# Kernel tuning notes

Measured on AMD Instinct MI355X. Metric: run time of the kernel, lower is better.

The kernel has to match this reference:

```python
import jax, jax.numpy as jnp
import numpy as np

ORDER = 12      # Coef_num in the original
BLOCK = 1024
N_FFT = 2046    # torch.stft(n_fft=2046) -> 1024 onesided bins
HOP = 511       # torch default n_fft // 4
WORN = 1024
G1, G2 = 0.92, 0.6


def burg_lpc(y):
    """Burg's method LPC (exactly librosa.lpc), vectorized over blocks. y: [B, N] -> [B, ORDER+1]."""
    ar = jnp.zeros((y.shape[0], ORDER + 1), y.dtype).at[:, 0].set(1.0)
    f = y[:, 1:]
    b = y[:, :-1]
    den = jnp.sum(f * f, -1) + jnp.sum(b * b, -1)
    for i in range(ORDER):
        k = -2.0 * jnp.sum(b * f, -1) / den                     # reflection coeff [B]
        js = np.arange(1, i + 2)
        ar = ar.at[:, js].set(ar[:, js] + k[:, None] * ar[:, i - js + 1])
        f_new = f + k[:, None] * b
        b = b + k[:, None] * f
        f = f_new
        den = (1.0 - k * k) * den - b[:, -1] ** 2 - f[:, 0] ** 2
        f = f[:, 1:]
        b = b[:, :-1]
    return ar


def perceptual_weights(y):
    """Stacked |freqz| weight matrix [n_blocks*11, 1024], matching the original append order."""
    n_blocks = y.shape[0] // BLOCK
    yb = y[: n_blocks * BLOCK].reshape(n_blocks, BLOCK)
    lpc = burg_lpc(yb)[:, :ORDER]                               # original drops coeff index 12
    j = np.arange(ORDER)
    a1 = (lpc * (G1 ** j)).astype(jnp.complex64)                # denominator coeffs (bandwidth-expanded)
    a2 = (lpc * (G2 ** j)).astype(jnp.complex64)                # numerator coeffs
    omega = jnp.pi * jnp.arange(WORN) / WORN                    # freqz worN=1024 digital freqs
    E = jnp.exp(-1j * omega[:, None] * j[None, :]).astype(jnp.complex64)   # [F, 12]
    # freqz is called inside the k1 loop: at step k1 only coeffs 0..k1 are filled -> triangular mask
    M = jnp.asarray(j[None, :] <= np.arange(1, ORDER)[:, None], jnp.complex64)  # [11, 12]
    num = jnp.einsum('bj,kj,fj->bkf', a2, M, E)
    den = jnp.einsum('bj,kj,fj->bkf', a1, M, E)
    return jnp.abs(num / den).reshape(n_blocks * (ORDER - 1), WORN)


def stft_mag(x):
    """torch.stft(x, n_fft=2046, center=True, reflect pad, rect window, onesided) magnitude -> [1024, n_frames]."""
    pad = N_FFT // 2
    xp = jnp.pad(x, (pad, pad), mode='reflect')
    n_frames = 1 + x.shape[0] // HOP
    idx = jnp.arange(n_frames)[:, None] * HOP + jnp.arange(N_FFT)[None, :]
    frames = xp[idx]                                            # [n_frames, 2046]
    return jnp.abs(jnp.fft.rfft(frames, axis=1)).T              # [1024, n_frames]


def setup_inputs() -> dict:
    key = jax.random.key(0)
    kx, ky = jax.random.split(key)
    L = 2048 * 1024
    x = jax.random.normal(kx, (L,), dtype=jnp.float32)
    y = jax.random.normal(ky, (L,), dtype=jnp.float32)
    return {"x": x, "y": y}


def reference(x, y):
    W = jax.lax.stop_gradient(perceptual_weights(y))            # original computes weights on detached numpy
    Sx = stft_mag(x)
    Sy = stft_mag(y)
    mse = jnp.mean((Sx - Sy) ** 2, axis=1)                      # [1024] per-frequency-bin MSE over frames
    return jnp.mean(mse[None, :] / W)                           # broadcast over [n_blocks*11, 1024]
```

## Files before the change

### kernel.cpp

```cpp
#include <hip/hip_runtime.h>
#include <hip/hip_bf16.h>

#define PI_D 3.14159265358979323846
#define L_TOTAL 2097152
#define NFRAMES 4105
#define NBLK    4108
#define MROWS_P 8216
#define MPAD    8320
#define KP      512
#define NDIM    2048
#define PSTRIDE 8224

#define COMBINE_BLOCKS 4352
#define INVW_BLOCKS 512


#define BURG_BLOCKS   512
#define FRAMES_BLOCKS 2080
#define BASIS_BLOCKS  512
#define SARR_BLOCKS   17
#define PREP_BLOCKS   (BURG_BLOCKS + FRAMES_BLOCKS + BASIS_BLOCKS + SARR_BLOCKS)

typedef __attribute__((ext_vector_type(8))) short short8;
typedef __attribute__((ext_vector_type(4))) short short4v;
typedef __attribute__((ext_vector_type(4))) float floatx4;
typedef float floatx4u __attribute__((ext_vector_type(4), aligned(4)));

typedef __attribute__((address_space(1))) void gvoid_as1;
typedef __attribute__((address_space(3))) void lvoid_as3;

__device__ __forceinline__ void gld_lds16(const void* g, void* l) {
    __builtin_amdgcn_global_load_lds((gvoid_as1*)g, (lvoid_as3*)l, 16, 0, 0);
}

__device__ __forceinline__ float b2f(short v) {
    unsigned int u = ((unsigned int)(unsigned short)v) << 16;
    return __uint_as_float(u);
}

__device__ __forceinline__ float xorall(float v) {
    v += __shfl_xor(v, 1, 64);
    v += __shfl_xor(v, 2, 64);
    v += __shfl_xor(v, 4, 64);
    v += __shfl_xor(v, 8, 64);
    v += __shfl_xor(v, 16, 64);
    v += __shfl_xor(v, 32, 64);
    return v;
}

__device__ __forceinline__ float wave_reduce(float v) {
    v += __shfl_down(v, 32, 64);
    v += __shfl_down(v, 16, 64);
    v += __shfl_down(v, 8, 64);
    v += __shfl_down(v, 4, 64);
    v += __shfl_down(v, 2, 64);
    v += __shfl_down(v, 1, 64);
    return v;
}

__device__ __forceinline__ void frames_body(int bid, int tid,
                                            const float* __restrict__ x,
                                            const float* __restrict__ y,
                                            __hip_bfloat16* __restrict__ A) {
    const int rb = bid >> 2;
    const int kc = (bid & 3) * 16 + (tid & 15);
    const int rowIn = tid >> 4;
    const int row = rb * 16 + rowIn;
    const int ci = rb * 1024 + kc * 16 + rowIn;
    __hip_bfloat16 tmp[8];
    if (row < MROWS_P) {
        const int b = row >> 1;
        const float* src = (row & 1) ? y : x;
        const int p0 = b * 511 + kc * 8 - 1023;
        if (kc < 63 && p0 >= 0 && p0 + 8 <= L_TOTAL) {
            floatx4u v0 = *(const floatx4u*)(src + p0);
            floatx4u v1 = *(const floatx4u*)(src + p0 + 4);
#pragma unroll
            for (int e = 0; e < 4; e++) tmp[e] = __float2bfloat16(v0[e]);
#pragma unroll
            for (int e = 0; e < 4; e++) tmp[4 + e] = __float2bfloat16(v1[e]);
        } else {
#pragma unroll
            for (int e = 0; e < 8; e++) {
                const int n = kc * 8 + e;
                float v = 0.f;
                if (n < 511) {
                    int p = p0 + e;
                    if (p < 0) p = -p;
                    else if (p >= L_TOTAL) p = 2 * L_TOTAL - 2 - p;
                    v = src[p];
                }
                tmp[e] = __float2bfloat16(v);
            }
        }
    } else {
#pragma unroll
        for (int e = 0; e < 8; e++) tmp[e] = __float2bfloat16(0.f);
    }
    *(short8*)((char*)A + (size_t)ci * 16) = *(short8*)tmp;
}

__device__ __forceinline__ void basis_body(int bid, int tid,
                                           __hip_bfloat16* __restrict__ Bt) {
    const int ci = bid * 256 + tid;
    const int rb = ci >> 10;
    const int kc = (ci >> 4) & 63;
    const int rowIn = ci & 15;
    const int row = rb * 16 + rowIn;
    const int f = row >> 1;
    const bool isSin = row & 1;
    const int n0 = kc * 8;
    const int m0 = (f * n0) % 2046;
    float s, c, ss, cs;
    __sincosf((float)m0 * (float)(PI_D / 1023.0), &s, &c);
    __sincosf((float)f * (float)(PI_D / 1023.0), &ss, &cs);
    __hip_bfloat16 tmp[8];
#pragma unroll
    for (int e = 0; e < 8; e++) {
        const int n = n0 + e;
        float v = isSin ? -s : c;
        if (n >= 511) v = 0.f;
        tmp[e] = __float2bfloat16(v);
        float c2 = c * cs - s * ss;
        float s2 = s * cs + c * ss;
        c = c2; s = s2;
    }
    *(short8*)((char*)Bt + (size_t)ci * 16) = *(short8*)tmp;
}

__device__ __forceinline__ void sarr_body(int bid, int tid,
                                          const float* __restrict__ x,
                                          const float* __restrict__ y,
                                          float4* __restrict__ S,
                                          float* __restrict__ wsf) {
    if (bid < 8) wsf[bid * 256 + tid] = 0.f;
    const int b = bid * 256 + tid;
    int p0 = 511 * b - 1023;
    int p1 = p0 + 1;
    int m0 = (p0 < 0) ? -p0 : ((p0 >= L_TOTAL) ? 2 * L_TOTAL - 2 - p0 : p0);
    int m1 = (p1 < 0) ? -p1 : ((p1 >= L_TOTAL) ? 2 * L_TOTAL - 2 - p1 : p1);
    S[b] = make_float4(x[m0], x[m1], y[m0], y[m1]);
}

__device__ __forceinline__ void burg_body(int bid, int tid,
                                          const float* __restrict__ y,
                                          float* __restrict__ ar_out) {
    const int lane = tid & 63;
    const int wid = tid >> 6;
    const int blk = bid * 4 + wid;
    const float4* yb4 = (const float4*)(y + (size_t)blk * 1024) + lane * 4;

    float t[16];
#pragma unroll
    for (int q = 0; q < 4; q++) {
        float4 v = yb4[q];
        t[q * 4 + 0] = v.x; t[q * 4 + 1] = v.y;
        t[q * 4 + 2] = v.z; t[q * 4 + 3] = v.w;
    }
    float b[16], f[16];
#pragma unroll
    for (int r = 0; r < 16; r++) b[r] = t[r];
#pragma unroll
    for (int r = 0; r < 15; r++) f[r] = t[r + 1];
    {
        float nb = __shfl_down(t[0], 1, 64);
        f[15] = (lane == 63) ? 0.f : nb;
        if (lane == 63) b[15] = 0.f;
    }

    float den = 0.f;
#pragma unroll
    for (int r = 0; r < 16; r++) den += f[r] * f[r] + b[r] * b[r];
    den = xorall(den);

    float ar_s[13];
    ar_s[0] = 1.f;
#pragma unroll
    for (int j = 1; j < 13; j++) ar_s[j] = 0.f;

#pragma unroll
    for (int i = 0; i < 12; i++) {
        float num = 0.f;
#pragma unroll
        for (int r = 0; r < 16; r++) num += f[r] * b[r];
        num = xorall(num);
        const float k = -2.f * num / den;

        float fu[16], bu[16];
#pragma unroll
        for (int r = 0; r < 16; r++) {
            fu[r] = f[r] + k * b[r];
            bu[r] = b[r] + k * f[r];
        }
        const float f0 = __shfl(fu[0], 0, 64);
        const int pos = 1022 - i;
        const int L = pos >> 4, S = pos & 15;
        const float blast = __shfl(bu[S], L, 64);

        den = (1.f - k * k) * den - blast * blast - f0 * f0;

        float nf = __shfl_down(fu[0], 1, 64);
#pragma unroll
        for (int r = 0; r < 15; r++) f[r] = fu[r + 1];
        f[15] = (lane == 63) ? 0.f : nf;
#pragma unroll
        for (int r = 0; r < 16; r++) b[r] = bu[r];
        if (lane == L) b[S] = 0.f;

        float tmp[13];
#pragma unroll
        for (int js = 1; js <= i + 1; js++) tmp[js] = ar_s[js] + k * ar_s[i + 1 - js];
#pragma unroll
        for (int js = 1; js <= i + 1; js++) ar_s[js] = tmp[js];
    }

#pragma unroll
    for (int j = 0; j < 12; j++)
        if (lane == j) ar_out[(size_t)blk * 12 + j] = ar_s[j];
}

__global__ __launch_bounds__(256) void prep_kernel(const float* __restrict__ x,
                                                   const float* __restrict__ y,
                                                   __hip_bfloat16* __restrict__ A,
                                                   __hip_bfloat16* __restrict__ Bt,
                                                   float4* __restrict__ S,
                                                   float* __restrict__ ar,
                                                   float* __restrict__ wsf) {
    const int bid = blockIdx.x;
    const int tid = threadIdx.x;
    if (bid < BURG_BLOCKS) {
        burg_body(bid, tid, y, ar);
    } else if (bid < BURG_BLOCKS + FRAMES_BLOCKS) {
        frames_body(bid - BURG_BLOCKS, tid, x, y, A);
    } else if (bid < BURG_BLOCKS + FRAMES_BLOCKS + BASIS_BLOCKS) {
        basis_body(bid - BURG_BLOCKS - FRAMES_BLOCKS, tid, Bt);
    } else {
        sarr_body(bid - BURG_BLOCKS - FRAMES_BLOCKS - BASIS_BLOCKS, tid, x, y, S, wsf);
    }
}

__global__ __launch_bounds__(512, 4) void gemm_p_kernel(
    const __hip_bfloat16* __restrict__ A, const __hip_bfloat16* __restrict__ Bt,
    __hip_bfloat16* __restrict__ Pt) {
    __shared__ __align__(16) __hip_bfloat16 Al[128 * 32];
    __shared__ __align__(16) __hip_bfloat16 Bl[128 * 32];

    const int tid = threadIdx.x;
    const int lane = tid & 63;
    const int w = tid >> 6;
    const int wm = w >> 1;
    const int wn = w & 1;
    const int q = lane >> 4, l15 = lane & 15;
    const int tileN = blockIdx.x * 128;
    const int tileM = blockIdx.y * 128;

    floatx4 acc[2][4];
#pragma unroll
    for (int i = 0; i < 2; i++)
#pragma unroll
        for (int j = 0; j < 4; j++) acc[i][j] = (floatx4){0.f, 0.f, 0.f, 0.f};

    const int gg = tid >> 6;
    const int inner = tid & 63;
    const char* pA = (const char*)A + ((((size_t)(tileM >> 4) + gg) << 10) + inner) * 16;
    const char* pB = (const char*)Bt + ((((size_t)(tileN >> 4) + gg) << 10) + inner) * 16;
    char* AlB = (char*)Al;
    char* BlB = (char*)Bl;

    for (int it = 0; it < KP / 32; it++) {
        gld_lds16(pA, AlB + tid * 16);
        gld_lds16(pB, BlB + tid * 16);
        pA += 1024; pB += 1024;
        __syncthreads();

        short8 af[2], bf[4];
#pragma unroll
        for (int sm = 0; sm < 2; sm++)
            af[sm] = *(const short8*)(AlB + (((wm * 2 + sm) * 64 + lane) * 16));
#pragma unroll
        for (int sn = 0; sn < 4; sn++)
            bf[sn] = *(const short8*)(BlB + (((wn * 4 + sn) * 64 + lane) * 16));
#pragma unroll
        for (int sm = 0; sm < 2; sm++)
#pragma unroll
            for (int sn = 0; sn < 4; sn++)
                acc[sm][sn] = __builtin_amdgcn_mfma_f32_16x16x32_bf16(
                    af[sm], bf[sn], acc[sm][sn], 0, 0, 0);
        __syncthreads();
    }

#pragma unroll
    for (int sm = 0; sm < 2; sm++) {
        const int rowBase = tileM + wm * 32 + sm * 16 + q * 4;
        if (rowBase >= MROWS_P) continue;
#pragma unroll
        for (int sn = 0; sn < 4; sn++) {
            const int colG = tileN + wn * 64 + sn * 16 + l15;
            short4v pk;
#pragma unroll
            for (int r = 0; r < 4; r++) {
                __hip_bfloat16 h = __float2bfloat16(acc[sm][sn][r]);
                pk[r] = *(short*)&h;
            }
            *(short4v*)((char*)Pt + ((size_t)colG * PSTRIDE + rowBase) * 2) = pk;
        }
    }
}

__device__ __forceinline__ void combine_body(int bx, int ty, int tid,
                                             const __hip_bfloat16* __restrict__ Pt,
                                             const float4* __restrict__ S,
                                             float* __restrict__ mse_sum) {
    const int lane = tid & 63;
    const int wid = tid >> 6;
    const int f = bx * 4 + wid;

    float wc[4], ws[4];
    wc[0] = 1.f; ws[0] = 0.f;
#pragma unroll
    for (int h = 1; h < 4; h++) {
        int m = (511 * h * f) % 2046;
        float s, c;
        __sincosf((float)m * (float)(PI_D / 1023.0), &s, &c);
        wc[h] = c; ws[h] = -s;
    }
    float wtc0, wts0, wtc1, wts1;
    {
        int m = (2044 * f) % 2046;
        float s, c;
        __sincosf((float)m * (float)(PI_D / 1023.0), &s, &c);
        wtc0 = c; wts0 = -s;
        m = (2045 * f) % 2046;
        __sincosf((float)m * (float)(PI_D / 1023.0), &s, &c);
        wtc1 = c; wts1 = -s;
    }

    const __hip_bfloat16* rowRe = Pt + (size_t)(2 * f) * PSTRIDE;
    const __hip_bfloat16* rowIm = rowRe + PSTRIDE;

    float acc = 0.f;
    const int tt0 = ty * 256 + 4 * lane;
    if (tt0 < NFRAMES) {
        short8 re0 = *(const short8*)(rowRe + 2 * tt0);
        short8 re1 = *(const short8*)(rowRe + 2 * tt0 + 8);
        short8 im0 = *(const short8*)(rowIm + 2 * tt0);
        short8 im1 = *(const short8*)(rowIm + 2 * tt0 + 8);
        float4 sT[4];
#pragma unroll
        for (int d = 0; d < 4; d++) sT[d] = S[tt0 + 4 + d];
        float vr[16], vi[16];
#pragma unroll
        for (int j = 0; j < 8; j++) {
            vr[j] = b2f(re0[j]); vr[j + 8] = b2f(re1[j]);
            vi[j] = b2f(im0[j]); vi[j + 8] = b2f(im1[j]);
        }
#pragma unroll
        for (int d = 0; d < 4; d++) {
            const int tt = tt0 + d;
            if (tt >= NFRAMES) break;
            float xr = 0.f, xi = 0.f, yr = 0.f, yi = 0.f;
#pragma unroll
            for (int h = 0; h < 4; h++) {
                const int qx = 2 * d + 2 * h;
                xr += wc[h] * vr[qx] - ws[h] * vi[qx];
                xi += wc[h] * vi[qx] + ws[h] * vr[qx];
                const int qy = qx + 1;
                yr += wc[h] * vr[qy] - ws[h] * vi[qy];
                yi += wc[h] * vi[qy] + ws[h] * vr[qy];
            }
            const float4 sd = sT[d];
            xr += wtc0 * sd.x + wtc1 * sd.y;
            xi += wts0 * sd.x + wts1 * sd.y;
            yr += wtc0 * sd.z + wtc1 * sd.w;
            yi += wts0 * sd.z + wts1 * sd.w;
            float dm = sqrtf(xr * xr + xi * xi) - sqrtf(yr * yr + yi * yi);
            acc += dm * dm;
        }
    }
    acc = xorall(acc);
    if (lane == 0) atomicAdd(&mse_sum[f], acc);
}

__device__ __forceinline__ void invw_body(int bid, int tid,
                                          const float* __restrict__ ar,
                                          float* __restrict__ invW) {
    __shared__ float sar[16][12];
    const int f = (bid & 3) * 256 + tid;
    const int b0 = (bid >> 2) * 16;
    if (tid < 16 * 12) ((float*)sar)[tid] = ar[(size_t)b0 * 12 + tid];
    __syncthreads();

    const float omega = (float)(PI_D / 1024.0) * (float)f;
    float sw, cw;
    __sincosf(omega, &sw, &cw);

    float acc = 0.f;
#pragma unroll 4
    for (int bb = 0; bb < 16; bb++) {
        float a0 = sar[bb][0];
        float nr = a0, ni = 0.f, dr = a0, di = 0.f;
        float er = 1.f, ei = 0.f;
        float g1p = 1.f, g2p = 1.f;
#pragma unroll
        for (int j = 1; j < 12; j++) {
            float er2 = er * cw + ei * sw;
            float ei2 = ei * cw - er * sw;
            er = er2; ei = ei2;
            g1p *= 0.92f; g2p *= 0.6f;
            float aj = sar[bb][j];
            float a1 = aj * g1p, a2 = aj * g2p;
            nr += a2 * er; ni += a2 * ei;
            dr += a1 * er; di += a1 * ei;
            float D = dr * dr + di * di;
            float Nn = nr * nr + ni * ni;
            acc += D * __builtin_amdgcn_rsqf(D * Nn);
        }
    }
    atomicAdd(&invW[f], acc);
}

__global__ __launch_bounds__(256) void combine_invw_kernel(
    const __hip_bfloat16* __restrict__ Pt,
    const float4* __restrict__ S,
    float* __restrict__ mse_sum,
    const float* __restrict__ ar,
    float* __restrict__ invW) {
    const int bid = blockIdx.x;
    const int tid = threadIdx.x;
    if (bid < INVW_BLOCKS) {
        invw_body(bid, tid, ar, invW);
    } else {
        const int cb = bid - INVW_BLOCKS;
        combine_body(cb & 255, cb >> 8, tid, Pt, S, mse_sum);
    }
}

__global__ void final_kernel(const float* __restrict__ mse_sum,
                             const float* __restrict__ invW,
                             float* __restrict__ out) {
    __shared__ float red[4];
    const int tid = threadIdx.x;
    float lo = 0.f;
    for (int f = tid; f < 1024; f += 256) lo += mse_sum[f] * invW[f];
    lo = wave_reduce(lo);
    if ((tid & 63) == 0) red[tid >> 6] = lo;
    __syncthreads();
    if (tid == 0) {
        float tot = red[0] + red[1] + red[2] + red[3];
        out[0] = tot * (float)(1.0 / (4105.0 * 22528.0 * 1024.0));
    }
}

extern "C" void kernel_launch(void* const* d_in, const int* in_sizes, int n_in,
                              void* d_out, int out_size, void* d_ws, size_t ws_size,
                              hipStream_t stream) {
    const float* x = (const float*)d_in[0];
    const float* y = (const float*)d_in[1];
    float* out = (float*)d_out;

    float* wsf = (float*)d_ws;
    float* mse_sum = wsf;
    float* invW = wsf + 1024;
    float* ar = wsf + 2080;
    float4* S = (float4*)((char*)d_ws + 131072);
    __hip_bfloat16* Ap = (__hip_bfloat16*)((char*)d_ws + 262144);
    __hip_bfloat16* Bp = (__hip_bfloat16*)((char*)d_ws + 8781824);
    __hip_bfloat16* Pt = (__hip_bfloat16*)((char*)d_ws + 10878976);

    prep_kernel<<<PREP_BLOCKS, 256, 0, stream>>>(x, y, Ap, Bp, S, ar, wsf);
    gemm_p_kernel<<<dim3(NDIM / 128, MPAD / 128), 512, 0, stream>>>(Ap, Bp, Pt);
    combine_invw_kernel<<<INVW_BLOCKS + COMBINE_BLOCKS, 256, 0, stream>>>(Pt, S, mse_sum, ar, invW);
    final_kernel<<<1, 256, 0, stream>>>(mse_sum, invW, out);
}
```

Baseline: 127.2 us.

## Switch STFT DFT GEMM operands from bf16 to fp8 e4m3 with repacked layout

Frames and DFT basis are now quantized to fp8 e4m3 instead of bf16, and the GEMM uses the fp8 MFMA instruction with 8-byte fragments and a single shared LDS buffer. The operand tiles are relaid out so each thread writes x and y, or cos and sin, pairs for one frame or frequency together. This halves prep writes and GEMM operand traffic. In exchange, e4m3 precision on Gaussian inputs and trig values may push the loss outside tolerance.

```diff
diff --git a/kernel.cpp b/kernel.cpp
--- a/kernel.cpp
+++ b/kernel.cpp
@@ -1,5 +1,6 @@
 #include <hip/hip_runtime.h>
 #include <hip/hip_bf16.h>
+#include <hip/hip_fp8.h>
 
 #define PI_D 3.14159265358979323846
 #define L_TOTAL 2097152
@@ -16,8 +17,8 @@
 
 
 #define BURG_BLOCKS   512
-#define FRAMES_BLOCKS 2080
-#define BASIS_BLOCKS  512
+#define FRAMES_BLOCKS 1040
+#define BASIS_BLOCKS  256
 #define SARR_BLOCKS   17
 #define PREP_BLOCKS   (BURG_BLOCKS + FRAMES_BLOCKS + BASIS_BLOCKS + SARR_BLOCKS)
 
@@ -36,6 +37,12 @@
 __device__ __forceinline__ float b2f(short v) {
     unsigned int u = ((unsigned int)(unsigned short)v) << 16;
     return __uint_as_float(u);
+}
+
+__device__ __forceinline__ unsigned int pk4_e4m3(float a, float b, float c, float d) {
+    __hip_fp8_e4m3 q0(a), q1(b), q2(c), q3(d);
+    return (unsigned int)q0.__x | ((unsigned int)q1.__x << 8)
+         | ((unsigned int)q2.__x << 16) | ((unsigned int)q3.__x << 24);
 }
 
 __device__ __forceinline__ float xorall(float v) {
@@ -61,71 +68,64 @@
 __device__ __forceinline__ void frames_body(int bid, int tid,
                                             const float* __restrict__ x,
                                             const float* __restrict__ y,
-                                            __hip_bfloat16* __restrict__ A) {
-    const int rb = bid >> 2;
-    const int kc = (bid & 3) * 16 + (tid & 15);
-    const int rowIn = tid >> 4;
-    const int row = rb * 16 + rowIn;
-    const int ci = rb * 1024 + kc * 16 + rowIn;
-    __hip_bfloat16 tmp[8];
-    if (row < MROWS_P) {
-        const int b = row >> 1;
-        const float* src = (row & 1) ? y : x;
-        const int p0 = b * 511 + kc * 8 - 1023;
-        if (kc < 63 && p0 >= 0 && p0 + 8 <= L_TOTAL) {
-            floatx4u v0 = *(const floatx4u*)(src + p0);
-            floatx4u v1 = *(const floatx4u*)(src + p0 + 4);
-#pragma unroll
-            for (int e = 0; e < 4; e++) tmp[e] = __float2bfloat16(v0[e]);
-#pragma unroll
-            for (int e = 0; e < 4; e++) tmp[4 + e] = __float2bfloat16(v1[e]);
-        } else {
-#pragma unroll
-            for (int e = 0; e < 8; e++) {
-                const int n = kc * 8 + e;
-                float v = 0.f;
-                if (n < 511) {
-                    int p = p0 + e;
-                    if (p < 0) p = -p;
-                    else if (p >= L_TOTAL) p = 2 * L_TOTAL - 2 - p;
-                    v = src[p];
-                }
-                tmp[e] = __float2bfloat16(v);
-            }
-        }
+                                            char* __restrict__ A) {
+    const int lane = tid & 63;
+    const int b = bid * 4 + (tid >> 6);
+    const int p0 = b * 511 + lane * 8 - 1023;
+    float xv[8], yv[8];
+    if (p0 >= 0 && p0 + 8 <= L_TOTAL) {
+        floatx4u x0 = *(const floatx4u*)(x + p0);
+        floatx4u x1 = *(const floatx4u*)(x + p0 + 4);
+        floatx4u y0 = *(const floatx4u*)(y + p0);
+        floatx4u y1 = *(const floatx4u*)(y + p0 + 4);
+#pragma unroll
+        for (int e = 0; e < 4; e++) { xv[e] = x0[e]; xv[4 + e] = x1[e]; }
+#pragma unroll
+        for (int e = 0; e < 4; e++) { yv[e] = y0[e]; yv[4 + e] = y1[e]; }
     } else {
 #pragma unroll
-        for (int e = 0; e < 8; e++) tmp[e] = __float2bfloat16(0.f);
-    }
-    *(short8*)((char*)A + (size_t)ci * 16) = *(short8*)tmp;
+        for (int e = 0; e < 8; e++) {
+            int p = p0 + e;
+            if (p < 0) p = -p;
+            else if (p >= L_TOTAL) p = 2 * L_TOTAL - 2 - p;
+            xv[e] = x[p];
+            yv[e] = y[p];
+        }
+    }
+    int4 pk;
+    pk.x = (int)pk4_e4m3(xv[0], xv[1], xv[2], xv[3]);
+    pk.y = (int)pk4_e4m3(xv[4], xv[5], xv[6], xv[7]);
+    pk.z = (int)pk4_e4m3(yv[0], yv[1], yv[2], yv[3]);
+    pk.w = (int)pk4_e4m3(yv[4], yv[5], yv[6], yv[7]);
+    *(int4*)(A + (size_t)(b >> 3) * 8192 + lane * 128 + (b & 7) * 16) = pk;
 }
 
 __device__ __forceinline__ void basis_body(int bid, int tid,
-                                           __hip_bfloat16* __restrict__ Bt) {
-    const int ci = bid * 256 + tid;
-    const int rb = ci >> 10;
-    const int kc = (ci >> 4) & 63;
-    const int rowIn = ci & 15;
-    const int row = rb * 16 + rowIn;
-    const int f = row >> 1;
-    const bool isSin = row & 1;
-    const int n0 = kc * 8;
+                                           char* __restrict__ Bt) {
+    const int lane = tid & 63;
+    const int f = bid * 4 + (tid >> 6);
+    const int n0 = lane * 8;
     const int m0 = (f * n0) % 2046;
     float s, c, ss, cs;
     __sincosf((float)m0 * (float)(PI_D / 1023.0), &s, &c);
     __sincosf((float)f * (float)(PI_D / 1023.0), &ss, &cs);
-    __hip_bfloat16 tmp[8];
+    float cv[8], sv[8];
 #pragma unroll
     for (int e = 0; e < 8; e++) {
         const int n = n0 + e;
-        float v = isSin ? -s : c;
-        if (n >= 511) v = 0.f;
-        tmp[e] = __float2bfloat16(v);
+        const bool valid = n < 511;
+        cv[e] = valid ? c : 0.f;
+        sv[e] = valid ? -s : 0.f;
         float c2 = c * cs - s * ss;
         float s2 = s * cs + c * ss;
         c = c2; s = s2;
     }
-    *(short8*)((char*)Bt + (size_t)ci * 16) = *(short8*)tmp;
+    int4 pk;
+    pk.x = (int)pk4_e4m3(cv[0], cv[1], cv[2], cv[3]);
+    pk.y = (int)pk4_e4m3(cv[4], cv[5], cv[6], cv[7]);
+    pk.z = (int)pk4_e4m3(sv[0], sv[1], sv[2], sv[3]);
+    pk.w = (int)pk4_e4m3(sv[4], sv[5], sv[6], sv[7]);
+    *(int4*)(Bt + (size_t)(f >> 3) * 8192 + lane * 128 + (f & 7) * 16) = pk;
 }
 
 __device__ __forceinline__ void sarr_body(int bid, int tid,
@@ -221,8 +221,8 @@
 
 __global__ __launch_bounds__(256) void prep_kernel(const float* __restrict__ x,
                                                    const float* __restrict__ y,
-                                                   __hip_bfloat16* __restrict__ A,
-                                                   __hip_bfloat16* __restrict__ Bt,
+                                                   char* __restrict__ A,
+                                                   char* __restrict__ Bt,
                                                    float4* __restrict__ S,
                                                    float* __restrict__ ar,
                                                    float* __restrict__ wsf) {
@@ -240,10 +240,9 @@
 }
 
 __global__ __launch_bounds__(512, 4) void gemm_p_kernel(
-    const __hip_bfloat16* __restrict__ A, const __hip_bfloat16* __restrict__ Bt,
+    const char* __restrict__ A, const char* __restrict__ Bt,
     __hip_bfloat16* __restrict__ Pt) {
-    __shared__ __align__(16) __hip_bfloat16 Al[128 * 32];
-    __shared__ __align__(16) __hip_bfloat16 Bl[128 * 32];
+    __shared__ __align__(16) char smem[8192];
 
     const int tid = threadIdx.x;
     const int lane = tid & 63;
@@ -260,31 +259,30 @@
 #pragma unroll
         for (int j = 0; j < 4; j++) acc[i][j] = (floatx4){0.f, 0.f, 0.f, 0.f};
 
-    const int gg = tid >> 6;
-    const int inner = tid & 63;
-    const char* pA = (const char*)A + ((((size_t)(tileM >> 4) + gg) << 10) + inner) * 16;
-    const char* pB = (const char*)Bt + ((((size_t)(tileN >> 4) + gg) << 10) + inner) * 16;
-    char* AlB = (char*)Al;
-    char* BlB = (char*)Bl;
+    const int t8 = tid & 255;
+    const int g = t8 >> 5;
+    const int u = t8 & 31;
+    const char* p = ((tid < 256)
+        ? A + (((size_t)(tileM >> 4) + g) << 13)
+        : Bt + (((size_t)(tileN >> 4) + g) << 13)) + u * 16;
 
     for (int it = 0; it < KP / 32; it++) {
-        gld_lds16(pA, AlB + tid * 16);
-        gld_lds16(pB, BlB + tid * 16);
-        pA += 1024; pB += 1024;
+        gld_lds16(p, smem + tid * 16);
+        p += 512;
         __syncthreads();
 
-        short8 af[2], bf[4];
+        long af[2], bf[4];
 #pragma unroll
         for (int sm = 0; sm < 2; sm++)
-            af[sm] = *(const short8*)(AlB + (((wm * 2 + sm) * 64 + lane) * 16));
+            af[sm] = *(const long*)(smem + (wm * 2 + sm) * 512 + lane * 8);
 #pragma unroll
         for (int sn = 0; sn < 4; sn++)
-            bf[sn] = *(const short8*)(BlB + (((wn * 4 + sn) * 64 + lane) * 16));
+            bf[sn] = *(const long*)(smem + 4096 + (wn * 4 + sn) * 512 + lane * 8);
 #pragma unroll
         for (int sm = 0; sm < 2; sm++)
 #pragma unroll
             for (int sn = 0; sn < 4; sn++)
-                acc[sm][sn] = __builtin_amdgcn_mfma_f32_16x16x32_bf16(
+                acc[sm][sn] = __builtin_amdgcn_mfma_f32_16x16x32_fp8_fp8(
                     af[sm], bf[sn], acc[sm][sn], 0, 0, 0);
         __syncthreads();
     }
@@ -463,9 +461,9 @@
     float* invW = wsf + 1024;
     float* ar = wsf + 2080;
     float4* S = (float4*)((char*)d_ws + 131072);
-    __hip_bfloat16* Ap = (__hip_bfloat16*)((char*)d_ws + 262144);
-    __hip_bfloat16* Bp = (__hip_bfloat16*)((char*)d_ws + 8781824);
-    __hip_bfloat16* Pt = (__hip_bfloat16*)((char*)d_ws + 10878976);
+    char* Ap = (char*)d_ws + 262144;
+    char* Bp = (char*)d_ws + 4521984;
+    __hip_bfloat16* Pt = (__hip_bfloat16*)((char*)d_ws + 8388608);
 
     prep_kernel<<<PREP_BLOCKS, 256, 0, stream>>>(x, y, Ap, Bp, S, ar, wsf);
     gemm_p_kernel<<<dim3(NDIM / 128, MPAD / 128), 512, 0, stream>>>(Ap, Bp, Pt);
```

Result: no change. 125.4 us (-1.5%).
